# Kernel tuning notes

Measured on AMD Instinct MI355X. Metric: run time of the kernel, lower is better.

The kernel has to match this reference:

```python
import jax, jax.numpy as jnp
import numpy as np

B, N, D, H = 2, 2048, 1024, 16
HD = D // H  # head_dim = 64
LN_EPS = 1e-5


def rotate_half(x):
    # x: [..., HD] with interleaved pairs -> (-x2, x1) interleaved back
    x = x.reshape(*x.shape[:-1], HD // 2, 2)
    x1, x2 = x[..., 0], x[..., 1]
    return jnp.stack((-x2, x1), axis=-1).reshape(*x.shape[:-2], HD)


def setup_inputs() -> dict:
    key = jax.random.key(0)
    ks = jax.random.split(key, 12)
    s = 0.02
    return {
        "descriptor": jax.random.normal(ks[0], (B, N, D), dtype=jnp.float32),
        "encoding": jax.random.normal(ks[1], (2, B, H, N, HD), dtype=jnp.float32),
        "w_qkv": s * jax.random.normal(ks[2], (3 * D, D), dtype=jnp.float32),
        "b_qkv": jnp.zeros((3 * D,), dtype=jnp.float32),
        "w_out": s * jax.random.normal(ks[3], (D, D), dtype=jnp.float32),
        "b_out": jnp.zeros((D,), dtype=jnp.float32),
        "w_ffn1": s * jax.random.normal(ks[4], (2 * D, 2 * D), dtype=jnp.float32),
        "b_ffn1": jnp.zeros((2 * D,), dtype=jnp.float32),
        "ln_g": jnp.ones((2 * D,), dtype=jnp.float32),
        "ln_b": jnp.zeros((2 * D,), dtype=jnp.float32),
        "w_ffn2": s * jax.random.normal(ks[5], (D, 2 * D), dtype=jnp.float32),
        "b_ffn2": jnp.zeros((D,), dtype=jnp.float32),
    }


def reference(descriptor, encoding, w_qkv, b_qkv, w_out, b_out,
              w_ffn1, b_ffn1, ln_g, ln_b, w_ffn2, b_ffn2):
    # fused QKV projection; last dim laid out as (H, HD, 3) like the torch code
    qkv = descriptor @ w_qkv.T + b_qkv                      # [B, N, 3D]
    qkv = qkv.reshape(B, N, H, HD, 3).transpose(0, 2, 1, 3, 4)  # [B, H, N, HD, 3]
    q, k, v = qkv[..., 0], qkv[..., 1], qkv[..., 2]

    # cached rotary embedding
    q = q * encoding[0] + rotate_half(q) * encoding[1]
    k = k * encoding[0] + rotate_half(k) * encoding[1]

    # scaled dot-product attention (no mask)
    scale = 1.0 / jnp.sqrt(jnp.asarray(HD, dtype=q.dtype))
    scores = jnp.einsum('bhqd,bhkd->bhqk', q, k) * scale    # [B, H, N, N]
    attn = jax.nn.softmax(scores, axis=-1)
    context = jnp.einsum('bhqk,bhkd->bhqd', attn, v)        # [B, H, N, HD]

    message = context.transpose(0, 2, 1, 3).reshape(B, N, D) @ w_out.T + b_out

    # concat-FFN: Linear -> LayerNorm -> GELU -> Linear
    h = jnp.concatenate([descriptor, message], axis=-1) @ w_ffn1.T + b_ffn1  # [B, N, 2D]
    mu = jnp.mean(h, axis=-1, keepdims=True)
    var = jnp.mean(jnp.square(h - mu), axis=-1, keepdims=True)
    h = (h - mu) * jax.lax.rsqrt(var + LN_EPS) * ln_g + ln_b
    h = jax.nn.gelu(h, approximate=False)
    return descriptor + h @ w_ffn2.T + b_ffn2
```

## Files before the change

### kernel.cpp

```cpp
#include <hip/hip_runtime.h>
#include <hip/hip_bf16.h>
#include <stdint.h>
#include <stddef.h>

#define B_   2
#define N_   2048
#define D_   1024
#define H_   16
#define HD_  64
#define BH_  (B_ * H_)
#define M_   (B_ * N_)

typedef short bf16x8 __attribute__((ext_vector_type(8)));
typedef float f32x4  __attribute__((ext_vector_type(4)));

static __device__ __forceinline__ unsigned short f2bf(float f) {
    union { float f; unsigned u; } c; c.f = f;
    unsigned r = (c.u + 0x7FFFu + ((c.u >> 16) & 1u)) >> 16;
    return (unsigned short)r;
}
static __device__ __forceinline__ float bf2f(unsigned short u) {
    union { unsigned u; float f; } c; c.u = ((unsigned)u) << 16; return c.f;
}

#define GLDS16(g, l)                                                                     \
    __builtin_amdgcn_global_load_lds((const __attribute__((address_space(1))) void*)(g), \
                                     (__attribute__((address_space(3))) void*)(l), 16, 0, 0)

#define QSCALE 0.18033688011112042f

__global__ __launch_bounds__(256) void k_cast_w4(const float* __restrict__ s0,
                                                 const float* __restrict__ s1,
                                                 const float* __restrict__ s2,
                                                 const float* __restrict__ s3,
                                                 unsigned short* __restrict__ d0,
                                                 unsigned short* __restrict__ d1,
                                                 unsigned short* __restrict__ d2,
                                                 unsigned short* __restrict__ d3) {
    int i = blockIdx.x * 256 + threadIdx.x;
    const float* s; unsigned short* d; int off;
    if (i < 786432)              { s = s0; d = d0; off = i; }
    else if (i < 1048576)        { s = s1; d = d1; off = i - 786432; }
    else if (i < 2097152)        { s = s2; d = d2; off = i - 1048576; }
    else                         { s = s3; d = d3; off = i - 2097152; }
    float4 v = *(const float4*)(s + (size_t)off * 4);
    ushort4 o;
    o.x = f2bf(v.x); o.y = f2bf(v.y); o.z = f2bf(v.z); o.w = f2bf(v.w);
    *(ushort4*)(d + (size_t)off * 4) = o;
}

__global__ __launch_bounds__(256) void k_cast_desc(const float* __restrict__ in,
                                                   unsigned short* __restrict__ cat) {
    int i = (blockIdx.x * 256 + threadIdx.x) * 4;
    float4 v = *(const float4*)(in + i);
    int row = i >> 10, col = i & 1023;
    ushort4 o;
    o.x = f2bf(v.x); o.y = f2bf(v.y); o.z = f2bf(v.z); o.w = f2bf(v.w);
    *(ushort4*)(cat + (size_t)row * 2048 + col) = o;
}

template <int EPI>
__global__ __launch_bounds__(256) void k_gemm(const unsigned short* __restrict__ A, int lda,
                                              const unsigned short* __restrict__ Bm, int ldb,
                                              void* __restrict__ Cv, int ldc,
                                              const float* __restrict__ bias,
                                              const float* __restrict__ resid, int ldr,
                                              unsigned short* __restrict__ qd,
                                              unsigned short* __restrict__ kd,
                                              unsigned short* __restrict__ vd,
                                              int K) {
    __shared__ unsigned short As[128 * 64];
    __shared__ unsigned short Bs[128 * 64];
    const int tid  = threadIdx.x;
    const int wave = tid >> 6, lane = tid & 63;
    const int wr = wave >> 1, wc = wave & 1;
    const int brow = blockIdx.y * 128, bcol = blockIdx.x * 128;

    const int srow = (lane >> 3);
    const int scol = (lane & 7) * 8;
    const int frow = lane & 15;
    const int fk   = (lane >> 4) * 8;

    f32x4 acc[4][4] = {};

    for (int kt = 0; kt < K; kt += 64) {
        __syncthreads();
#pragma unroll
        for (int j = 0; j < 4; ++j) {
            int r = wave * 32 + j * 8 + srow;
            GLDS16(A  + (size_t)(brow + r) * lda + kt + scol, (char*)As + wave * 4096 + j * 1024);
            GLDS16(Bm + (size_t)(bcol + r) * ldb + kt + scol, (char*)Bs + wave * 4096 + j * 1024);
        }
        __syncthreads();
#pragma unroll
        for (int ks = 0; ks < 2; ++ks) {
            bf16x8 a[4], b[4];
#pragma unroll
            for (int m = 0; m < 4; ++m)
                a[m] = *(const bf16x8*)(As + (wr * 64 + m * 16 + frow) * 64 + ks * 32 + fk);
#pragma unroll
            for (int n = 0; n < 4; ++n)
                b[n] = *(const bf16x8*)(Bs + (wc * 64 + n * 16 + frow) * 64 + ks * 32 + fk);
#pragma unroll
            for (int m = 0; m < 4; ++m)
#pragma unroll
                for (int n = 0; n < 4; ++n)
                    acc[m][n] = __builtin_amdgcn_mfma_f32_16x16x32_bf16(a[m], b[n], acc[m][n], 0, 0, 0);
        }
    }

    const int orow = (lane >> 4) * 4;
#pragma unroll
    for (int m = 0; m < 4; ++m) {
        int row0 = brow + wr * 64 + m * 16 + orow;
#pragma unroll
        for (int n = 0; n < 4; ++n) {
            int col = bcol + wc * 64 + n * 16 + frow;
            float bs = bias[col];
#pragma unroll
            for (int r = 0; r < 4; ++r) {
                float v = acc[m][n][r] + bs;
                if (EPI == 3) {
                    int row = row0 + r;
                    int bb = row >> 11, nr = row & (N_ - 1);
                    int h = col / 192;
                    int rem = col - h * 192;
                    int d = rem / 3;
                    int c = rem - d * 3;
                    unsigned short* dst = (c == 0) ? qd : (c == 1) ? kd : vd;
                    dst[(((size_t)(bb * H_ + h)) * N_ + nr) * 64 + d] = f2bf(v);
                } else if (EPI == 2) {
                    v += resid[(size_t)(row0 + r) * ldr + col];
                    ((float*)Cv)[(size_t)(row0 + r) * ldc + col] = v;
                } else {
                    ((unsigned short*)Cv)[(size_t)(row0 + r) * ldc + col] = f2bf(v);
                }
            }
        }
    }
}

__global__ __launch_bounds__(256) void k_rope_ip(unsigned short* __restrict__ Qb,
                                                 unsigned short* __restrict__ Kb,
                                                 const float* __restrict__ enc) {
    int idx = blockIdx.x * 256 + threadIdx.x;
    int i  = idx & 31;
    int n  = (idx >> 5) & (N_ - 1);
    int bh = idx >> 16;
    size_t eoff = ((size_t)bh * N_ + n) * 64 + i * 2;
    float2 e0 = *(const float2*)(enc + eoff);
    float2 e1 = *(const float2*)(enc + (size_t)BH_ * N_ * 64 + eoff);
    ushort2 qp = *(const ushort2*)(Qb + eoff);
    ushort2 kp = *(const ushort2*)(Kb + eoff);
    float q1 = bf2f(qp.x), q2 = bf2f(qp.y);
    float k1 = bf2f(kp.x), k2 = bf2f(kp.y);
    ushort2 qo, ko;
    qo.x = f2bf((q1 * e0.x - q2 * e1.x) * QSCALE);
    qo.y = f2bf((q2 * e0.y + q1 * e1.y) * QSCALE);
    ko.x = f2bf(k1 * e0.x - k2 * e1.x);
    ko.y = f2bf(k2 * e0.y + k1 * e1.y);
    *(ushort2*)(Qb + eoff) = qo;
    *(ushort2*)(Kb + eoff) = ko;
}

__global__ __launch_bounds__(256) void k_transpose_v(const unsigned short* __restrict__ Vb,
                                                     unsigned short* __restrict__ Vt) {
    __shared__ unsigned short t[64][72];
    int bh = blockIdx.y, n0 = blockIdx.x * 64;
    int tid = threadIdx.x;
    int r  = tid >> 2;
    int c0 = (tid & 3) * 16;
    const unsigned short* src = Vb + ((size_t)bh * N_ + n0 + r) * 64 + c0;
    *(bf16x8*)(&t[r][c0])     = *(const bf16x8*)(src);
    *(bf16x8*)(&t[r][c0 + 8]) = *(const bf16x8*)(src + 8);
    __syncthreads();
    int d  = tid >> 2;
    int nc = (tid & 3) * 16;
    bf16x8 o0, o1;
#pragma unroll
    for (int j = 0; j < 8; ++j) { o0[j] = (short)t[nc + j][d]; o1[j] = (short)t[nc + 8 + j][d]; }
    unsigned short* dst = Vt + ((size_t)bh * 64 + d) * N_ + n0 + nc;
    *(bf16x8*)(dst)     = o0;
    *(bf16x8*)(dst + 8) = o1;
}

__global__ __launch_bounds__(256) void k_attn(const unsigned short* __restrict__ Qb,
                                              const unsigned short* __restrict__ Kb,
                                              const unsigned short* __restrict__ Vt,
                                              unsigned short* __restrict__ Ctx) {
    __shared__ unsigned short Ks[2][64 * 64];
    __shared__ unsigned short Vs[2][64 * 64];
    __shared__ unsigned short Ps[4][16 * 64];

    int lin = blockIdx.x + 32 * blockIdx.y;
    int ixc = lin >> 3;
    int bh  = (lin & 7) * 4 + (ixc >> 5);
    int q0  = (ixc & 31) * 64;
    int b = bh >> 4, h = bh & 15;
    int tid = threadIdx.x, wave = tid >> 6, lane = tid & 63;
    int frow = lane & 15, fk = (lane >> 4) * 8, g = lane >> 4;
    int f7x8 = (frow & 7) * 8;

    int srow = lane >> 3;
    int scol = ((lane & 7) ^ srow) * 8;

    const unsigned short* Kbh = Kb + (size_t)bh * N_ * 64;
    const unsigned short* Vbh = Vt + (size_t)bh * 64 * N_;

#define ATTN_STAGE(bufi, kt)                                                           \
    do {                                                                               \
        _Pragma("unroll")                                                              \
        for (int j = 0; j < 2; ++j) {                                                  \
            int rr = wave * 16 + j * 8 + srow;                                         \
            GLDS16(Kbh + (size_t)((kt) + rr) * 64 + scol,                              \
                   (char*)Ks[bufi] + wave * 2048 + j * 1024);                          \
            GLDS16(Vbh + (size_t)rr * N_ + (kt) + scol,                                \
                   (char*)Vs[bufi] + wave * 2048 + j * 1024);                          \
        }                                                                              \
    } while (0)

    const unsigned short* qptr = Qb + ((size_t)bh * N_ + q0 + wave * 16 + frow) * 64;
    bf16x8 qf[2];
    qf[0] = *(const bf16x8*)(qptr + fk);
    qf[1] = *(const bf16x8*)(qptr + 32 + fk);

    float m = -INFINITY;
    float l = 0.f;
    f32x4 accO[4] = {};

    ATTN_STAGE(0, 0);

    for (int t = 0; t < N_ / 64; ++t) {
        int cur = t & 1;
        __syncthreads();
        if (t + 1 < N_ / 64) ATTN_STAGE(cur ^ 1, (t + 1) * 64);

        f32x4 st[4];
        __builtin_amdgcn_s_setprio(1);
#pragma unroll
        for (int kc = 0; kc < 4; ++kc) {
            f32x4 a = {};
#pragma unroll
            for (int ks = 0; ks < 2; ++ks) {
                bf16x8 kfr = *(const bf16x8*)(Ks[cur] + (kc * 16 + frow) * 64 + ((ks * 32 + fk) ^ f7x8));
                a = __builtin_amdgcn_mfma_f32_16x16x32_bf16(kfr, qf[ks], a, 0, 0, 0);
            }
            st[kc] = a;
        }
        __builtin_amdgcn_s_setprio(0);

        float mloc = fmaxf(fmaxf(fmaxf(st[0][0], st[0][1]), fmaxf(st[0][2], st[0][3])),
                           fmaxf(fmaxf(st[1][0], st[1][1]), fmaxf(st[1][2], st[1][3])));
        mloc = fmaxf(mloc,
               fmaxf(fmaxf(fmaxf(st[2][0], st[2][1]), fmaxf(st[2][2], st[2][3])),
                     fmaxf(fmaxf(st[3][0], st[3][1]), fmaxf(st[3][2], st[3][3]))));
        mloc = fmaxf(mloc, __shfl_xor(mloc, 16));
        mloc = fmaxf(mloc, __shfl_xor(mloc, 32));
        float mn = fmaxf(m, mloc);
        float sc = exp2f(m - mn);
        m = mn;
        float ps = 0.f;
#pragma unroll
        for (int kc = 0; kc < 4; ++kc)
#pragma unroll
            for (int r = 0; r < 4; ++r) {
                float p = exp2f(st[kc][r] - mn);
                st[kc][r] = p;
                ps += p;
            }
        ps += __shfl_xor(ps, 16);
        ps += __shfl_xor(ps, 32);
        l = l * sc + ps;

        float scl[4];
#pragma unroll
        for (int r = 0; r < 4; ++r) scl[r] = __shfl(sc, g * 4 + r);
#pragma unroll
        for (int df = 0; df < 4; ++df)
#pragma unroll
            for (int r = 0; r < 4; ++r) accO[df][r] *= scl[r];

#pragma unroll
        for (int kc = 0; kc < 4; ++kc) {
            unsigned lo, hi;
            asm("v_cvt_pk_bf16_f32 %0, %1, %2" : "=v"(lo) : "v"(st[kc][0]), "v"(st[kc][1]));
            asm("v_cvt_pk_bf16_f32 %0, %1, %2" : "=v"(hi) : "v"(st[kc][2]), "v"(st[kc][3]));
            int col = (kc * 16 + g * 4) ^ f7x8;
            uint2 w; w.x = lo; w.y = hi;
            *(uint2*)(&Ps[wave][frow * 64 + col]) = w;
        }
        asm volatile("s_waitcnt lgkmcnt(0)" ::: "memory");
        __builtin_amdgcn_sched_barrier(0);

        __builtin_amdgcn_s_setprio(1);
#pragma unroll
        for (int ks = 0; ks < 2; ++ks) {
            bf16x8 pa = *(const bf16x8*)(&Ps[wave][frow * 64 + ((ks * 32 + fk) ^ f7x8)]);
#pragma unroll
            for (int df = 0; df < 4; ++df) {
                bf16x8 vf = *(const bf16x8*)(Vs[cur] + (df * 16 + frow) * 64 + ((ks * 32 + fk) ^ f7x8));
                accO[df] = __builtin_amdgcn_mfma_f32_16x16x32_bf16(pa, vf, accO[df], 0, 0, 0);
            }
        }
        __builtin_amdgcn_s_setprio(0);
    }

    float inv[4];
#pragma unroll
    for (int r = 0; r < 4; ++r) inv[r] = 1.0f / __shfl(l, g * 4 + r);
#pragma unroll
    for (int df = 0; df < 4; ++df)
#pragma unroll
        for (int r = 0; r < 4; ++r) {
            int q = q0 + wave * 16 + g * 4 + r;
            Ctx[((size_t)(b * N_ + q)) * D_ + h * 64 + df * 16 + frow] = f2bf(accO[df][r] * inv[r]);
        }
#undef ATTN_STAGE
}

__global__ __launch_bounds__(256) void k_ln_gelu(const unsigned short* __restrict__ hsrc,
                                                 const float* __restrict__ gma,
                                                 const float* __restrict__ bta,
                                                 unsigned short* __restrict__ out) {
    __shared__ float red[2][4];
    int row = blockIdx.x, tid = threadIdx.x;
    const unsigned short* hr = hsrc + (size_t)row * 2048 + tid * 8;
    bf16x8 hv = *(const bf16x8*)(hr);
    float xs[8];
    float s = 0.f, q = 0.f;
#pragma unroll
    for (int j = 0; j < 8; ++j) {
        float x = bf2f((unsigned short)hv[j]);
        xs[j] = x; s += x; q += x * x;
    }
#pragma unroll
    for (int off = 1; off < 64; off <<= 1) {
        s += __shfl_xor(s, off);
        q += __shfl_xor(q, off);
    }
    int wave = tid >> 6;
    if ((tid & 63) == 0) { red[0][wave] = s; red[1][wave] = q; }
    __syncthreads();
    s = red[0][0] + red[0][1] + red[0][2] + red[0][3];
    q = red[1][0] + red[1][1] + red[1][2] + red[1][3];
    float mu   = s * (1.f / 2048.f);
    float var  = q * (1.f / 2048.f) - mu * mu;
    float rstd = rsqrtf(var + 1e-5f);
    int c = tid * 8;
#pragma unroll
    for (int j = 0; j < 8; ++j) {
        float x = (xs[j] - mu) * rstd * gma[c + j] + bta[c + j];
        float y = 0.5f * x * (1.f + erff(x * 0.70710678118654752f));
        out[(size_t)row * 2048 + c + j] = f2bf(y);
    }
}

extern "C" void kernel_launch(void* const* d_in, const int* in_sizes, int n_in,
                              void* d_out, int out_size, void* d_ws, size_t ws_size,
                              hipStream_t stream) {
    const float* descriptor = (const float*)d_in[0];
    const float* encoding   = (const float*)d_in[1];
    const float* w_qkv      = (const float*)d_in[2];
    const float* b_qkv      = (const float*)d_in[3];
    const float* w_out      = (const float*)d_in[4];
    const float* b_out      = (const float*)d_in[5];
    const float* w_ffn1     = (const float*)d_in[6];
    const float* b_ffn1     = (const float*)d_in[7];
    const float* ln_g       = (const float*)d_in[8];
    const float* ln_b       = (const float*)d_in[9];
    const float* w_ffn2     = (const float*)d_in[10];
    const float* b_ffn2     = (const float*)d_in[11];
    float* out = (float*)d_out;

    char* ws = (char*)d_ws;
    unsigned short* wffn1_b = (unsigned short*)(ws);
    unsigned short* wffn2_b = (unsigned short*)(ws + ((size_t)8  << 20));
    unsigned short* wout_b  = (unsigned short*)(ws + ((size_t)12 << 20));
    unsigned short* cat     = (unsigned short*)(ws + ((size_t)14 << 20));
    unsigned short* Qb      = (unsigned short*)(ws + ((size_t)30 << 20));
    unsigned short* Kb      = (unsigned short*)(ws + ((size_t)38 << 20));
    unsigned short* Vb      = (unsigned short*)(ws + ((size_t)46 << 20));
    unsigned short* wqkv_b  = (unsigned short*)(ws + ((size_t)54 << 20));
    unsigned short* Vt      = (unsigned short*)(ws + ((size_t)54 << 20));
    unsigned short* msg     = (unsigned short*)(ws + ((size_t)46 << 20));
    unsigned short* hbuf    = (unsigned short*)(ws + ((size_t)30 << 20));
    unsigned short* h2      = (unsigned short*)(ws + ((size_t)14 << 20));

    k_cast_desc<<<4096, 256, 0, stream>>>(descriptor, cat);
    k_cast_w4<<<10240, 256, 0, stream>>>(w_qkv, w_out, w_ffn1, w_ffn2,
                                         wqkv_b, wout_b, wffn1_b, wffn2_b);

    k_gemm<3><<<dim3(24, 32), 256, 0, stream>>>(cat, 2048, wqkv_b, 1024, nullptr, 0,
                                                b_qkv, nullptr, 0, Qb, Kb, Vb, 1024);
    k_rope_ip<<<8192, 256, 0, stream>>>(Qb, Kb, encoding);
    k_transpose_v<<<dim3(32, 32), 256, 0, stream>>>(Vb, Vt);
    k_attn<<<dim3(32, 32), 256, 0, stream>>>(Qb, Kb, Vt, msg);
    k_gemm<1><<<dim3(8, 32), 256, 0, stream>>>(msg, 1024, wout_b, 1024, cat + 1024, 2048,
                                               b_out, nullptr, 0, nullptr, nullptr, nullptr, 1024);
    k_gemm<1><<<dim3(16, 32), 256, 0, stream>>>(cat, 2048, wffn1_b, 2048, hbuf, 2048,
                                                b_ffn1, nullptr, 0, nullptr, nullptr, nullptr, 2048);
    k_ln_gelu<<<4096, 256, 0, stream>>>(hbuf, ln_g, ln_b, h2);
    k_gemm<2><<<dim3(8, 32), 256, 0, stream>>>(h2, 2048, wffn2_b, 2048, out, 1024,
                                               b_ffn2, descriptor, 1024, nullptr, nullptr, nullptr, 2048);
}
```

Before: 455.1 us.

## Double-buffer GEMM LDS tiles and skip softmax rescale when max grows little

```diff
diff --git a/kernel.cpp b/kernel.cpp
--- a/kernel.cpp
+++ b/kernel.cpp
@@ -69,8 +69,8 @@
                                               unsigned short* __restrict__ kd,
                                               unsigned short* __restrict__ vd,
                                               int K) {
-    __shared__ unsigned short As[128 * 64];
-    __shared__ unsigned short Bs[128 * 64];
+    __shared__ unsigned short As[2][128 * 64];
+    __shared__ unsigned short Bs[2][128 * 64];
     const int tid  = threadIdx.x;
     const int wave = tid >> 6, lane = tid & 63;
     const int wr = wave >> 1, wc = wave & 1;
@@ -83,24 +83,33 @@
 
     f32x4 acc[4][4] = {};
 
-    for (int kt = 0; kt < K; kt += 64) {
+#define GEMM_STAGE(bufi, kt)                                                              \
+    do {                                                                                  \
+        _Pragma("unroll")                                                                 \
+        for (int j = 0; j < 4; ++j) {                                                     \
+            int r = wave * 32 + j * 8 + srow;                                             \
+            GLDS16(A  + (size_t)(brow + r) * lda + (kt) + scol,                           \
+                   (char*)As[bufi] + wave * 4096 + j * 1024);                             \
+            GLDS16(Bm + (size_t)(bcol + r) * ldb + (kt) + scol,                           \
+                   (char*)Bs[bufi] + wave * 4096 + j * 1024);                             \
+        }                                                                                 \
+    } while (0)
+
+    GEMM_STAGE(0, 0);
+    const int nt = K >> 6;
+    for (int t = 0; t < nt; ++t) {
+        int cur = t & 1;
         __syncthreads();
-#pragma unroll
-        for (int j = 0; j < 4; ++j) {
-            int r = wave * 32 + j * 8 + srow;
-            GLDS16(A  + (size_t)(brow + r) * lda + kt + scol, (char*)As + wave * 4096 + j * 1024);
-            GLDS16(Bm + (size_t)(bcol + r) * ldb + kt + scol, (char*)Bs + wave * 4096 + j * 1024);
-        }
-        __syncthreads();
+        if (t + 1 < nt) GEMM_STAGE(cur ^ 1, (t + 1) * 64);
 #pragma unroll
         for (int ks = 0; ks < 2; ++ks) {
             bf16x8 a[4], b[4];
 #pragma unroll
             for (int m = 0; m < 4; ++m)
-                a[m] = *(const bf16x8*)(As + (wr * 64 + m * 16 + frow) * 64 + ks * 32 + fk);
+                a[m] = *(const bf16x8*)(As[cur] + (wr * 64 + m * 16 + frow) * 64 + ks * 32 + fk);
 #pragma unroll
             for (int n = 0; n < 4; ++n)
-                b[n] = *(const bf16x8*)(Bs + (wc * 64 + n * 16 + frow) * 64 + ks * 32 + fk);
+                b[n] = *(const bf16x8*)(Bs[cur] + (wc * 64 + n * 16 + frow) * 64 + ks * 32 + fk);
 #pragma unroll
             for (int m = 0; m < 4; ++m)
 #pragma unroll
@@ -108,6 +117,7 @@
                     acc[m][n] = __builtin_amdgcn_mfma_f32_16x16x32_bf16(a[m], b[n], acc[m][n], 0, 0, 0);
         }
     }
+#undef GEMM_STAGE
 
     const int orow = (lane >> 4) * 4;
 #pragma unroll
@@ -256,29 +266,43 @@
                      fmaxf(fmaxf(st[3][0], st[3][1]), fmaxf(st[3][2], st[3][3]))));
         mloc = fmaxf(mloc, __shfl_xor(mloc, 16));
         mloc = fmaxf(mloc, __shfl_xor(mloc, 32));
-        float mn = fmaxf(m, mloc);
-        float sc = exp2f(m - mn);
-        m = mn;
-        float ps = 0.f;
-#pragma unroll
-        for (int kc = 0; kc < 4; ++kc)
-#pragma unroll
-            for (int r = 0; r < 4; ++r) {
-                float p = exp2f(st[kc][r] - mn);
-                st[kc][r] = p;
-                ps += p;
-            }
-        ps += __shfl_xor(ps, 16);
-        ps += __shfl_xor(ps, 32);
-        l = l * sc + ps;
-
-        float scl[4];
-#pragma unroll
-        for (int r = 0; r < 4; ++r) scl[r] = __shfl(sc, g * 4 + r);
-#pragma unroll
-        for (int df = 0; df < 4; ++df)
-#pragma unroll
-            for (int r = 0; r < 4; ++r) accO[df][r] *= scl[r];
+        if (__all(mloc <= m + 8.0f)) {
+            float ps = 0.f;
+#pragma unroll
+            for (int kc = 0; kc < 4; ++kc)
+#pragma unroll
+                for (int r = 0; r < 4; ++r) {
+                    float p = exp2f(st[kc][r] - m);
+                    st[kc][r] = p;
+                    ps += p;
+                }
+            ps += __shfl_xor(ps, 16);
+            ps += __shfl_xor(ps, 32);
+            l += ps;
+        } else {
+            float mn = fmaxf(m, mloc);
+            float sc = exp2f(m - mn);
+            m = mn;
+            float ps = 0.f;
+#pragma unroll
+            for (int kc = 0; kc < 4; ++kc)
+#pragma unroll
+                for (int r = 0; r < 4; ++r) {
+                    float p = exp2f(st[kc][r] - mn);
+                    st[kc][r] = p;
+                    ps += p;
+                }
+            ps += __shfl_xor(ps, 16);
+            ps += __shfl_xor(ps, 32);
+            l = l * sc + ps;
+            float scl[4];
+#pragma unroll
+            for (int r = 0; r < 4; ++r) scl[r] = __shfl(sc, g * 4 + r);
+#pragma unroll
+            for (int df = 0; df < 4; ++df)
+#pragma unroll
+                for (int r = 0; r < 4; ++r) accO[df][r] *= scl[r];
+        }
 
 #pragma unroll
         for (int kc = 0; kc < 4; ++kc) {
```

After: 465.6 us. +2.3%, slower.
